# Kernel optimization log

Hardware: AMD Instinct MI355X
Metric: run time of the kernel (lower is better)

Reference implementation:

```python
import jax, jax.numpy as jnp
import numpy as np
from jax import lax

TD_MAX = 2000
STRIDE = 100


def setup_inputs() -> dict:
    key = jax.random.key(0)
    x = jax.random.normal(key, (20000, 512, 3), dtype=jnp.float32)
    return {"x": x}


def reference(x) -> jnp.ndarray:
    # x: [T, N, 3] trajectory (2D input would be reshaped to [T, -1, 3])
    if x.ndim == 2:
        x = x.reshape(x.shape[0], -1, 3)
    T = x.shape[0]
    N3 = x.shape[1] * x.shape[2]
    t0s = jnp.arange(0, T - TD_MAX, STRIDE)  # time origins, stride 100

    def step(msd, t0):
        # window of td_max frames starting at t0: [td_max, N, 3]
        w = lax.dynamic_slice(x, (t0, 0, 0), (TD_MAX, x.shape[1], x.shape[2]))
        d = w - w[0]                       # displacement from origin frame
        msd = msd + jnp.sum(d * d, axis=(1, 2)) / N3
        return msd, None

    msd0 = jnp.zeros((TD_MAX,), dtype=x.dtype)
    msd, _ = lax.scan(step, msd0, t0s)
    return msd / t0s.shape[0]
```

## Files before the change

### kernel.cpp

```cpp
#include <hip/hip_runtime.h>


typedef __attribute__((ext_vector_type(8))) short bf16x8;
typedef __attribute__((ext_vector_type(4))) short bf16x4;
typedef __attribute__((ext_vector_type(4))) float f32x4;

#define ROWF   1536
#define NFRAME 20000
#define NORIG  180
#define WIN    20
#define FB     32
#define NFB    625
#define NKC    4
#define KC     384
#define NKS    12
#define TDMAX  2000
#define PLANE  (NORIG * TDMAX)
#define SOFF   (NKC * PLANE)
#define LROW   392
#define SCALE  (1.0f / (1536.0f * 180.0f))

static __device__ __forceinline__ short f2bf(float f) {
    unsigned u = __builtin_bit_cast(unsigned, f);
    u += 0x7fffu + ((u >> 16) & 1u);
    return (short)(u >> 16);
}

static __device__ __forceinline__ bf16x4 pack4(const float4& v) {
    bf16x4 r;
    r[0] = f2bf(v.x); r[1] = f2bf(v.y); r[2] = f2bf(v.z); r[3] = f2bf(v.w);
    return r;
}

__global__ __launch_bounds__(256)
void msd_s_kernel(const float* __restrict__ x, float* __restrict__ S) {
    const int t    = blockIdx.x * 4 + (threadIdx.x >> 6);
    const int lane = threadIdx.x & 63;
    const float* p = x + (size_t)t * ROWF + lane * 4;
    float a = 0.0f;
    #pragma unroll
    for (int k = 0; k < 6; ++k) {
        const float4 v = *(const float4*)(p + k * 256);
        a += v.x*v.x + v.y*v.y + v.z*v.z + v.w*v.w;
    }
    #pragma unroll
    for (int off = 32; off >= 1; off >>= 1)
        a += __shfl_xor(a, off, 64);
    if (lane == 0) S[t] = a;
}

__global__ __launch_bounds__(256)
void msd_dot_kernel(const float* __restrict__ x, float* __restrict__ ws) {
    __shared__ short lA[FB * LROW];
    __shared__ short lB[FB * LROW];

    const int fb  = blockIdx.x >> 2;
    const int kc  = blockIdx.x & 3;
    const int t0  = fb * FB;
    const int tid = threadIdx.x;

    const int cmin = t0 / 100;
    int iBase = cmin - (WIN - 1); if (iBase < 0) iBase = 0;

    #pragma unroll
    for (int it = 0; it < 12; ++it) {
        const unsigned seg = it * 256 + tid;
        const unsigned r   = seg / 96u;
        const unsigned c4  = seg % 96u;
        const float4 v = *(const float4*)(x + (size_t)(t0 + r) * ROWF
                                            + kc * KC + c4 * 4);
        *(bf16x4*)&lA[r * LROW + c4 * 4] = pack4(v);
    }
    #pragma unroll
    for (int it = 0; it < 12; ++it) {
        const unsigned seg = it * 256 + tid;
        const unsigned r   = seg / 96u;
        const unsigned c4  = seg % 96u;
        int iNom = iBase + (int)r;
        int iClp = (iNom < NORIG) ? iNom : (NORIG - 1);
        const float4 v = *(const float4*)(x + (size_t)(iClp * 100) * ROWF
                                            + kc * KC + c4 * 4);
        *(bf16x4*)&lB[r * LROW + c4 * 4] = pack4(v);
    }
    __syncthreads();

    const int lane = tid & 63;
    const int w    = tid >> 6;
    const int mt   = w >> 1;
    const int nt   = w & 1;
    const int m    = lane & 15;
    const int quad = lane >> 4;

    const short* pa = &lA[(16 * mt + m) * LROW + quad * 8];
    const short* pb = &lB[(16 * nt + m) * LROW + quad * 8];

    f32x4 acc = {};
    #pragma unroll
    for (int ks = 0; ks < NKS; ++ks) {
        acc = __builtin_amdgcn_mfma_f32_16x16x32_bf16(*(const bf16x8*)(pa + ks * 32),
                                                      *(const bf16x8*)(pb + ks * 32),
                                                      acc, 0, 0, 0);
    }

    float* wsp = ws + (size_t)kc * PLANE;
    #pragma unroll
    for (int r = 0; r < 4; ++r) {
        const int j  = 16 * mt + quad * 4 + r;
        const int tt = t0 + j;
        const int c  = tt / 100;
        const int i  = iBase + 16 * nt + m;
        const int k  = c - i;
        if (k >= 0 && k < WIN && i < NORIG) {
            const int td = tt - 100 * i;
            wsp[(size_t)i * TDMAX + td] = acc[r];
        }
    }
}

__global__ __launch_bounds__(256)
void msd_reduce_kernel(const float* __restrict__ ws, float* __restrict__ out) {
    __shared__ float red[4][64];
    const int lane = threadIdx.x & 63;
    const int w    = threadIdx.x >> 6;
    const int td   = blockIdx.x * 64 + lane;
    const int tdc  = (td < TDMAX) ? td : (TDMAX - 1);
    const float* S = ws + SOFF;

    float accS = 0.0f, accD = 0.0f;
    #pragma unroll 5
    for (int i = w * 45; i < w * 45 + 45; ++i) {
        accS += S[100 * i + tdc] + S[100 * i];
        const float* p = ws + (size_t)i * TDMAX + tdc;
        accD += p[0] + p[PLANE] + p[2 * PLANE] + p[3 * PLANE];
    }
    red[w][lane] = accS - 2.0f * accD;
    __syncthreads();
    if (w == 0 && td < TDMAX)
        out[td] = (red[0][lane] + red[1][lane] + red[2][lane] + red[3][lane]) * SCALE;
}

extern "C" void kernel_launch(void* const* d_in, const int* in_sizes, int n_in,
                              void* d_out, int out_size, void* d_ws, size_t ws_size,
                              hipStream_t stream) {
    const float* x = (const float*)d_in[0];
    float* out = (float*)d_out;
    float* ws  = (float*)d_ws;

    msd_s_kernel<<<NFRAME / 4, 256, 0, stream>>>(x, ws + SOFF);
    msd_dot_kernel<<<NFB * NKC, 256, 0, stream>>>(x, ws);
    msd_reduce_kernel<<<(TDMAX + 63) / 64, 256, 0, stream>>>(ws, out);
}
```

Baseline: 202.1 us.

## Fuse squared-norm computation into dot kernel's tile load and drop separate pass

The separate kernel that reads all of x to compute per-frame squared norms is removed. The dot kernel now computes partial squared norms for each of the four column chunks while loading its A tile, with an 8-lane shuffle reduction. The reduce kernel sums the four partial norms per frame. This avoids a second full read of the 123 MB input and one kernel launch, at the cost of extra loads in the reduce kernel. The load mapping also changes to one row per 8 threads with strided columns.

```diff
diff --git a/kernel.cpp b/kernel.cpp
--- a/kernel.cpp
+++ b/kernel.cpp
@@ -33,23 +33,6 @@
 }
 
 __global__ __launch_bounds__(256)
-void msd_s_kernel(const float* __restrict__ x, float* __restrict__ S) {
-    const int t    = blockIdx.x * 4 + (threadIdx.x >> 6);
-    const int lane = threadIdx.x & 63;
-    const float* p = x + (size_t)t * ROWF + lane * 4;
-    float a = 0.0f;
-    #pragma unroll
-    for (int k = 0; k < 6; ++k) {
-        const float4 v = *(const float4*)(p + k * 256);
-        a += v.x*v.x + v.y*v.y + v.z*v.z + v.w*v.w;
-    }
-    #pragma unroll
-    for (int off = 32; off >= 1; off >>= 1)
-        a += __shfl_xor(a, off, 64);
-    if (lane == 0) S[t] = a;
-}
-
-__global__ __launch_bounds__(256)
 void msd_dot_kernel(const float* __restrict__ x, float* __restrict__ ws) {
     __shared__ short lA[FB * LROW];
     __shared__ short lB[FB * LROW];
@@ -62,25 +45,36 @@
     const int cmin = t0 / 100;
     int iBase = cmin - (WIN - 1); if (iBase < 0) iBase = 0;
 
-    #pragma unroll
-    for (int it = 0; it < 12; ++it) {
-        const unsigned seg = it * 256 + tid;
-        const unsigned r   = seg / 96u;
-        const unsigned c4  = seg % 96u;
-        const float4 v = *(const float4*)(x + (size_t)(t0 + r) * ROWF
-                                            + kc * KC + c4 * 4);
-        *(bf16x4*)&lA[r * LROW + c4 * 4] = pack4(v);
+    {
+        const int r  = tid >> 3;
+        const int c8 = tid & 7;
+        const float* src = x + (size_t)(t0 + r) * ROWF + kc * KC + c8 * 4;
+        short* dst = &lA[r * LROW + c8 * 4];
+        float sq = 0.0f;
+        #pragma unroll
+        for (int it = 0; it < 12; ++it) {
+            const float4 v = *(const float4*)(src + it * 32);
+            sq += v.x*v.x + v.y*v.y + v.z*v.z + v.w*v.w;
+            *(bf16x4*)(dst + it * 32) = pack4(v);
+        }
+        sq += __shfl_xor(sq, 1, 64);
+        sq += __shfl_xor(sq, 2, 64);
+        sq += __shfl_xor(sq, 4, 64);
+        if (c8 == 0)
+            ws[SOFF + (size_t)kc * NFRAME + t0 + r] = sq;
     }
-    #pragma unroll
-    for (int it = 0; it < 12; ++it) {
-        const unsigned seg = it * 256 + tid;
-        const unsigned r   = seg / 96u;
-        const unsigned c4  = seg % 96u;
-        int iNom = iBase + (int)r;
-        int iClp = (iNom < NORIG) ? iNom : (NORIG - 1);
-        const float4 v = *(const float4*)(x + (size_t)(iClp * 100) * ROWF
-                                            + kc * KC + c4 * 4);
-        *(bf16x4*)&lB[r * LROW + c4 * 4] = pack4(v);
+    {
+        const int r  = tid >> 3;
+        const int c8 = tid & 7;
+        const int iNom = iBase + r;
+        const int iClp = (iNom < NORIG) ? iNom : (NORIG - 1);
+        const float* src = x + (size_t)(iClp * 100) * ROWF + kc * KC + c8 * 4;
+        short* dst = &lB[r * LROW + c8 * 4];
+        #pragma unroll
+        for (int it = 0; it < 12; ++it) {
+            const float4 v = *(const float4*)(src + it * 32);
+            *(bf16x4*)(dst + it * 32) = pack4(v);
+        }
     }
     __syncthreads();
 
@@ -124,16 +118,25 @@
     const int w    = threadIdx.x >> 6;
     const int td   = blockIdx.x * 64 + lane;
     const int tdc  = (td < TDMAX) ? td : (TDMAX - 1);
-    const float* S = ws + SOFF;
+    const float* Sp = ws + SOFF;
 
-    float accS = 0.0f, accD = 0.0f;
+    float acc = 0.0f;
     #pragma unroll 5
     for (int i = w * 45; i < w * 45 + 45; ++i) {
-        accS += S[100 * i + tdc] + S[100 * i];
+        const int t = 100 * i + tdc;
+        const float St = Sp[t]
+                       + Sp[1 * NFRAME + t]
+                       + Sp[2 * NFRAME + t]
+                       + Sp[3 * NFRAME + t];
+        const float Si = Sp[100 * i]
+                       + Sp[1 * NFRAME + 100 * i]
+                       + Sp[2 * NFRAME + 100 * i]
+                       + Sp[3 * NFRAME + 100 * i];
         const float* p = ws + (size_t)i * TDMAX + tdc;
-        accD += p[0] + p[PLANE] + p[2 * PLANE] + p[3 * PLANE];
+        const float d = p[0] + p[PLANE] + p[2 * PLANE] + p[3 * PLANE];
+        acc += St + Si - 2.0f * d;
     }
-    red[w][lane] = accS - 2.0f * accD;
+    red[w][lane] = acc;
     __syncthreads();
     if (w == 0 && td < TDMAX)
         out[td] = (red[0][lane] + red[1][lane] + red[2][lane] + red[3][lane]) * SCALE;
@@ -146,7 +149,6 @@
     float* out = (float*)d_out;
     float* ws  = (float*)d_ws;
 
-    msd_s_kernel<<<NFRAME / 4, 256, 0, stream>>>(x, ws + SOFF);
     msd_dot_kernel<<<NFB * NKC, 256, 0, stream>>>(x, ws);
     msd_reduce_kernel<<<(TDMAX + 63) / 64, 256, 0, stream>>>(ws, out);
 }
```

Measured after the change: 192.6 us. 4.7% less time.
